# Kernel optimization log

Measured on AMD Instinct MI355X. Metric: run time of the kernel, lower is better.

## Reference

```python
import jax, jax.numpy as jnp
import numpy as np

N = 50000        # nodes
E = 800000       # edges
IN_FEAT = 128
OUT_FEAT = 64
HEADS = 4
NUM_CLASSES = 40
NEG_SLOPE = 0.2  # DGL GATConv default


def setup_inputs() -> dict:
    key = jax.random.key(0)
    ks = jax.random.split(key, 12)
    x = jax.random.normal(ks[0], (N, IN_FEAT), dtype=jnp.float32)
    src = jax.random.randint(ks[1], (E,), 0, N, dtype=jnp.int32)
    dst = jax.random.randint(ks[2], (E,), 0, N, dtype=jnp.int32)
    # layer 1 params: fc W1 [in, H*D], attn_l/attn_r [H, D], bias [H*D]
    s1 = 1.0 / np.sqrt(IN_FEAT)
    W1 = jax.random.normal(ks[3], (IN_FEAT, HEADS * OUT_FEAT), dtype=jnp.float32) * s1
    al1 = jax.random.normal(ks[4], (HEADS, OUT_FEAT), dtype=jnp.float32) * 0.1
    ar1 = jax.random.normal(ks[5], (HEADS, OUT_FEAT), dtype=jnp.float32) * 0.1
    b1 = jnp.zeros((HEADS * OUT_FEAT,), dtype=jnp.float32)
    # layer 2 params: fc W2 [H*D, C], attn [1, C], bias [C]
    hid = HEADS * OUT_FEAT
    s2 = 1.0 / np.sqrt(hid)
    W2 = jax.random.normal(ks[6], (hid, NUM_CLASSES), dtype=jnp.float32) * s2
    al2 = jax.random.normal(ks[7], (1, NUM_CLASSES), dtype=jnp.float32) * 0.1
    ar2 = jax.random.normal(ks[8], (1, NUM_CLASSES), dtype=jnp.float32) * 0.1
    b2 = jnp.zeros((NUM_CLASSES,), dtype=jnp.float32)
    return {"x": x, "src": src, "dst": dst,
            "W1": W1, "al1": al1, "ar1": ar1, "b1": b1,
            "W2": W2, "al2": al2, "ar2": ar2, "b2": b2}


def gat_layer(x, W, al, ar, bias, src, dst, heads, out_feat):
    n = x.shape[0]
    h = (x @ W).reshape(n, heads, out_feat)            # [N,H,D]
    el = jnp.sum(h * al[None], axis=-1)                # [N,H]
    er = jnp.sum(h * ar[None], axis=-1)                # [N,H]
    e = el[src] + er[dst]                              # [E,H]
    e = jnp.where(e > 0, e, NEG_SLOPE * e)             # LeakyReLU
    # segment softmax over edges sharing the same destination
    emax = jax.ops.segment_max(e, dst, num_segments=n)           # [N,H]
    emax = jnp.where(jnp.isfinite(emax), emax, 0.0)              # isolated nodes
    ee = jnp.exp(e - emax[dst])                                  # [E,H]
    denom = jax.ops.segment_sum(ee, dst, num_segments=n)         # [N,H]
    denom = jnp.where(denom > 0, denom, 1.0)
    alpha = ee / denom[dst]                                      # [E,H]
    msg = h[src] * alpha[:, :, None]                             # [E,H,D]
    out = jax.ops.segment_sum(msg, dst, num_segments=n)          # [N,H,D]
    return out + bias.reshape(1, heads, out_feat)


def reference(x, src, dst, W1, al1, ar1, b1, W2, al2, ar2, b2):
    h = gat_layer(x, W1, al1, ar1, b1, src, dst, HEADS, OUT_FEAT)  # [N,H,D]
    h = h.reshape(h.shape[0], HEADS * OUT_FEAT)
    h = jax.nn.elu(h)
    h = gat_layer(h, W2, al2, ar2, b2, src, dst, 1, NUM_CLASSES)   # [N,1,C]
    return jnp.squeeze(h, axis=1)                                   # [N,C]
```

## Files before the change

### kernel.cpp

```cpp
#include <hip/hip_runtime.h>

#define NN 50000
#define NE 800000
#define HID 256
#define NCLS 40

typedef short bf16x8 __attribute__((ext_vector_type(8)));
typedef float f32x4 __attribute__((ext_vector_type(4)));

__device__ inline unsigned short f2bf(float f) {
    unsigned int u = __float_as_uint(f);
    return (unsigned short)((u + 0x7FFFu + ((u >> 16) & 1u)) >> 16);
}
__device__ inline unsigned int pack2bf(float a, float b) {
    return (unsigned int)f2bf(a) | ((unsigned int)f2bf(b) << 16);
}
__device__ inline float2 bf2x(unsigned int u) {
    return make_float2(__uint_as_float(u << 16), __uint_as_float(u & 0xFFFF0000u));
}

__global__ void k_count(const int* __restrict__ dst, int* __restrict__ counts) {
    int e = blockIdx.x * 256 + threadIdx.x;
    if (e < NE) atomicAdd(&counts[dst[e]], 1);
}

__global__ void k_scanA(const int* __restrict__ counts, int* __restrict__ indptr,
                        int* __restrict__ bsum) {
    __shared__ int sh[256];
    int t = threadIdx.x;
    int idx = blockIdx.x * 256 + t;
    int c = idx < NN ? counts[idx] : 0;
    sh[t] = c;
    __syncthreads();
    for (int off = 1; off < 256; off <<= 1) {
        int v = (t >= off) ? sh[t - off] : 0;
        __syncthreads();
        sh[t] += v;
        __syncthreads();
    }
    if (idx < NN) indptr[idx] = sh[t] - c;
    if (t == 255) bsum[blockIdx.x] = sh[255];
}

__global__ void k_scanB(int* __restrict__ bsum, int nb) {
    __shared__ int sh[256];
    int t = threadIdx.x;
    int c = t < nb ? bsum[t] : 0;
    sh[t] = c;
    __syncthreads();
    for (int off = 1; off < 256; off <<= 1) {
        int v = (t >= off) ? sh[t - off] : 0;
        __syncthreads();
        sh[t] += v;
        __syncthreads();
    }
    if (t < nb) bsum[t] = sh[t] - c;
}

__global__ void k_scanC(int* __restrict__ indptr, const int* __restrict__ bsum,
                        int* __restrict__ fill) {
    int idx = blockIdx.x * 256 + threadIdx.x;
    if (idx < NN) {
        indptr[idx] += bsum[idx >> 8];
        fill[idx] = 0;
    }
    if (idx == 0) indptr[NN] = NE;
}

__global__ void k_scatterw(const int* __restrict__ src, const int* __restrict__ dst,
                           const int* __restrict__ indptr, int* __restrict__ fill,
                           const float* __restrict__ el1, const float* __restrict__ er1,
                           int* __restrict__ srcs, float4* __restrict__ w4) {
    int e = blockIdx.x * 256 + threadIdx.x;
    if (e < NE) {
        int d = dst[e];
        int s = src[e];
        int pos = atomicAdd(&fill[d], 1);
        int j = indptr[d] + pos;
        srcs[j] = s;
        float4 ls = *(const float4*)&el1[(size_t)s * 4];
        float4 rd = *(const float4*)&er1[(size_t)d * 4];
        float e0 = ls.x + rd.x, e1 = ls.y + rd.y, e2 = ls.z + rd.z, e3 = ls.w + rd.w;
        e0 = e0 > 0.f ? e0 : 0.2f * e0;
        e1 = e1 > 0.f ? e1 : 0.2f * e1;
        e2 = e2 > 0.f ? e2 : 0.2f * e2;
        e3 = e3 > 0.f ? e3 : 0.2f * e3;
        w4[j] = make_float4(__expf(e0), __expf(e1), __expf(e2), __expf(e3));
    }
}

__global__ void k_prep(const float* __restrict__ W1, const float* __restrict__ al,
                       const float* __restrict__ ar, const float* __restrict__ W2,
                       float* __restrict__ wel, float* __restrict__ wer,
                       unsigned short* __restrict__ W1Tb,
                       unsigned short* __restrict__ W2Tb) {
    int gid = blockIdx.x * 256 + threadIdx.x;
    int nth = gridDim.x * 256;
    const int TOT = 512 + 32768 + 48 * 256;
    for (int i = gid; i < TOT; i += nth) {
        if (i < 512) {
            int k = i >> 2, h = i & 3;
            float a = 0.f, b = 0.f;
            for (int dd = 0; dd < 64; ++dd) {
                float w = W1[k * 256 + h * 64 + dd];
                a = fmaf(w, al[h * 64 + dd], a);
                b = fmaf(w, ar[h * 64 + dd], b);
            }
            wel[i] = a;
            wer[i] = b;
        } else if (i < 512 + 32768) {
            int j = i - 512;
            int col = j >> 7, k = j & 127;
            W1Tb[j] = f2bf(W1[k * 256 + col]);
        } else {
            int j = i - 512 - 32768;
            int col = j >> 8, kk = j & 255;
            W2Tb[j] = (col < NCLS) ? f2bf(W2[kk * 40 + col]) : (unsigned short)0;
        }
    }
}

__global__ void k_elr1x(const float* __restrict__ x, const float* __restrict__ wel,
                        const float* __restrict__ wer, float* __restrict__ el1,
                        float* __restrict__ er1, unsigned short* __restrict__ xb) {
    __shared__ float xs[64 * 129];
    __shared__ float wels[512], wers[512];
    int t = threadIdx.x;
    int n0 = blockIdx.x * 64;
    wels[t] = wel[t]; wels[256 + t] = wel[256 + t];
    wers[t] = wer[t]; wers[256 + t] = wer[256 + t];
    for (int i = 0; i < 8; ++i) {
        int f = i * 256 + t;
        int row = f >> 5;
        int col4 = (f & 31) * 4;
        float4 v = make_float4(0.f, 0.f, 0.f, 0.f);
        if (n0 + row < NN) v = ((const float4*)x)[(size_t)n0 * 32 + f];
        xs[row * 129 + col4 + 0] = v.x;
        xs[row * 129 + col4 + 1] = v.y;
        xs[row * 129 + col4 + 2] = v.z;
        xs[row * 129 + col4 + 3] = v.w;
    }
    __syncthreads();
    int node = t & 63;
    int h = t >> 6;
    float a = 0.f, b = 0.f;
    for (int k = 0; k < 128; ++k) {
        float xv = xs[node * 129 + k];
        a = fmaf(xv, wels[k * 4 + h], a);
        b = fmaf(xv, wers[k * 4 + h], b);
    }
    if (n0 + node < NN) {
        el1[(size_t)(n0 + node) * 4 + h] = a;
        er1[(size_t)(n0 + node) * 4 + h] = b;
    }
    for (int i = 0; i < 4; ++i) {
        int g = (i * 256 + t) * 8;
        int row = g >> 7, col = g & 127;
        if (n0 + row < NN) {
            ushort4 lo, hi;
            lo.x = f2bf(xs[row * 129 + col + 0]);
            lo.y = f2bf(xs[row * 129 + col + 1]);
            lo.z = f2bf(xs[row * 129 + col + 2]);
            lo.w = f2bf(xs[row * 129 + col + 3]);
            hi.x = f2bf(xs[row * 129 + col + 4]);
            hi.y = f2bf(xs[row * 129 + col + 5]);
            hi.z = f2bf(xs[row * 129 + col + 6]);
            hi.w = f2bf(xs[row * 129 + col + 7]);
            *(ushort4*)&xb[(size_t)(n0 + row) * 128 + col] = lo;
            *(ushort4*)&xb[(size_t)(n0 + row) * 128 + col + 4] = hi;
        }
    }
}

#define XG_STRIDE 260
#define EB_STRIDE 264
#define FMA8(AC0, AC1, AC2, AC3, WQ, XV) \
    AC0.x = fmaf(WQ.x, XV.x, AC0.x); AC0.y = fmaf(WQ.x, XV.y, AC0.y); \
    AC1.x = fmaf(WQ.y, XV.x, AC1.x); AC1.y = fmaf(WQ.y, XV.y, AC1.y); \
    AC2.x = fmaf(WQ.z, XV.x, AC2.x); AC2.y = fmaf(WQ.z, XV.y, AC2.y); \
    AC3.x = fmaf(WQ.w, XV.x, AC3.x); AC3.y = fmaf(WQ.w, XV.y, AC3.y);

__global__ void k_agg1m(const unsigned int* __restrict__ xb32,
                        const float4* __restrict__ w4,
                        const int* __restrict__ indptr, const int* __restrict__ srcs,
                        const unsigned short* __restrict__ W1Tb,
                        const unsigned short* __restrict__ W2Tb,
                        const float* __restrict__ b1,
                        const float* __restrict__ al2, const float* __restrict__ ar2,
                        unsigned short* __restrict__ h2b,
                        float* __restrict__ el2, float* __restrict__ er2) {
    __shared__ unsigned int xg[16 * XG_STRIDE];
    __shared__ __align__(16) unsigned char pool[10496];
    float4 (*sw)[64] = (float4(*)[64])pool;
    int (*si)[64] = (int(*)[64])(pool + 8192);
    unsigned short* eb = (unsigned short*)pool;
    float* pel = (float*)(pool + 8448);
    float* per_ = (float*)(pool + 8640);
    int t = threadIdx.x;
    int wv = t >> 6, l = t & 63;
    int n0 = blockIdx.x * 16;
    int d0 = n0 + wv * 4;
    int ip[5];
#pragma unroll
    for (int q = 0; q < 5; ++q) ip[q] = indptr[d0 + q];
    int w2 = wv * 2;
#pragma unroll
    for (int p = 0; p < 2; ++p) {
        int begA = ip[2 * p + 0], endA = ip[2 * p + 1];
        int begB = ip[2 * p + 1], endB = ip[2 * p + 2];
        int degA = endA - begA, degB = endB - begB;
        int sA = 0, sB = 0;
        float4 wA = make_float4(0.f, 0.f, 0.f, 0.f);
        float4 wB = make_float4(0.f, 0.f, 0.f, 0.f);
        if (l < degA) { sA = srcs[begA + l]; wA = w4[begA + l]; }
        if (l < degB) { sB = srcs[begB + l]; wB = w4[begB + l]; }
        si[w2 + 0][l] = sA; sw[w2 + 0][l] = wA;
        si[w2 + 1][l] = sB; sw[w2 + 1][l] = wB;
        float2 aA0 = {0,0}, aA1 = {0,0}, aA2 = {0,0}, aA3 = {0,0};
        float2 aB0 = {0,0}, aB1 = {0,0}, aB2 = {0,0}, aB3 = {0,0};
        int capA = degA < 64 ? degA : 64;
        int capB = degB < 64 ? degB : 64;
        int mcap = capA > capB ? capA : capB;
        for (int e = 0; e < mcap; e += 8) {
            unsigned int uA[8], uB[8];
            bool doA = e < capA, doB = e < capB;
            if (doA) {
#pragma unroll
                for (int q = 0; q < 8; ++q)
                    uA[q] = xb32[(size_t)si[w2][e + q] * 64 + l];
            }
            if (doB) {
#pragma unroll
                for (int q = 0; q < 8; ++q)
                    uB[q] = xb32[(size_t)si[w2 + 1][e + q] * 64 + l];
            }
            if (doA) {
#pragma unroll
                for (int q = 0; q < 8; ++q) {
                    float4 wq = sw[w2][e + q];
                    float2 xv = bf2x(uA[q]);
                    FMA8(aA0, aA1, aA2, aA3, wq, xv)
                }
            }
            if (doB) {
#pragma unroll
                for (int q = 0; q < 8; ++q) {
                    float4 wq = sw[w2 + 1][e + q];
                    float2 xv = bf2x(uB[q]);
                    FMA8(aB0, aB1, aB2, aB3, wq, xv)
                }
            }
        }
        for (int j = begA + 64; j < endA; ++j) {
            float4 wq = w4[j];
            float2 xv = bf2x(xb32[(size_t)srcs[j] * 64 + l]);
            FMA8(aA0, aA1, aA2, aA3, wq, xv)
        }
        for (int j = begB + 64; j < endB; ++j) {
            float4 wq = w4[j];
            float2 xv = bf2x(xb32[(size_t)srcs[j] * 64 + l]);
            FMA8(aB0, aB1, aB2, aB3, wq, xv)
        }
        float dA0 = wA.x, dA1 = wA.y, dA2 = wA.z, dA3 = wA.w;
        float dB0 = wB.x, dB1 = wB.y, dB2 = wB.z, dB3 = wB.w;
        for (int j = begA + 64 + l; j < endA; j += 64) {
            float4 wt = w4[j];
            dA0 += wt.x; dA1 += wt.y; dA2 += wt.z; dA3 += wt.w;
        }
        for (int j = begB + 64 + l; j < endB; j += 64) {
            float4 wt = w4[j];
            dB0 += wt.x; dB1 += wt.y; dB2 += wt.z; dB3 += wt.w;
        }
#pragma unroll
        for (int off = 32; off > 0; off >>= 1) {
            dA0 += __shfl_xor(dA0, off); dA1 += __shfl_xor(dA1, off);
            dA2 += __shfl_xor(dA2, off); dA3 += __shfl_xor(dA3, off);
            dB0 += __shfl_xor(dB0, off); dB1 += __shfl_xor(dB1, off);
            dB2 += __shfl_xor(dB2, off); dB3 += __shfl_xor(dB3, off);
        }
        float iA0 = dA0 > 0.f ? 1.f / dA0 : 0.f;
        float iA1 = dA1 > 0.f ? 1.f / dA1 : 0.f;
        float iA2 = dA2 > 0.f ? 1.f / dA2 : 0.f;
        float iA3 = dA3 > 0.f ? 1.f / dA3 : 0.f;
        float iB0 = dB0 > 0.f ? 1.f / dB0 : 0.f;
        float iB1 = dB1 > 0.f ? 1.f / dB1 : 0.f;
        float iB2 = dB2 > 0.f ? 1.f / dB2 : 0.f;
        float iB3 = dB3 > 0.f ? 1.f / dB3 : 0.f;
        unsigned int* xgA = &xg[(wv * 4 + 2 * p + 0) * XG_STRIDE];
        xgA[0 * 64 + l] = pack2bf(aA0.x * iA0, aA0.y * iA0);
        xgA[1 * 64 + l] = pack2bf(aA1.x * iA1, aA1.y * iA1);
        xgA[2 * 64 + l] = pack2bf(aA2.x * iA2, aA2.y * iA2);
        xgA[3 * 64 + l] = pack2bf(aA3.x * iA3, aA3.y * iA3);
        unsigned int* xgB = &xg[(wv * 4 + 2 * p + 1) * XG_STRIDE];
        xgB[0 * 64 + l] = pack2bf(aB0.x * iB0, aB0.y * iB0);
        xgB[1 * 64 + l] = pack2bf(aB1.x * iB1, aB1.y * iB1);
        xgB[2 * 64 + l] = pack2bf(aB2.x * iB2, aB2.y * iB2);
        xgB[3 * 64 + l] = pack2bf(aB3.x * iB3, aB3.y * iB3);
    }
    __syncthreads();
    int lrow = l & 15, lk = l >> 4;
    {
        f32x4 acc[4] = {};
#pragma unroll
        for (int kt = 0; kt < 4; ++kt) {
            bf16x8 av = *(const bf16x8*)&xg[lrow * XG_STRIDE + wv * 64 + kt * 16 + lk * 4];
#pragma unroll
            for (int nt = 0; nt < 4; ++nt) {
                int col = wv * 64 + nt * 16 + lrow;
                bf16x8 bv = *(const bf16x8*)&W1Tb[(size_t)col * 128 + kt * 32 + lk * 8];
                acc[nt] = __builtin_amdgcn_mfma_f32_16x16x32_bf16(av, bv, acc[nt], 0, 0, 0);
            }
        }
#pragma unroll
        for (int nt = 0; nt < 4; ++nt) {
            int col = wv * 64 + nt * 16 + lrow;
            float bv1 = b1[col];
#pragma unroll
            for (int r = 0; r < 4; ++r) {
                int rloc = lk * 4 + r;
                float o = acc[nt][r] + bv1;
                o = o > 0.f ? o : (__expf(o) - 1.f);
                eb[rloc * EB_STRIDE + col] = f2bf(o);
            }
        }
    }
    __syncthreads();
    if (wv < 3) {
        f32x4 acc2 = {};
#pragma unroll
        for (int kt = 0; kt < 8; ++kt) {
            bf16x8 av = *(const bf16x8*)&eb[lrow * EB_STRIDE + kt * 32 + lk * 8];
            bf16x8 bv = *(const bf16x8*)&W2Tb[(size_t)(wv * 16 + lrow) * 256 + kt * 32 + lk * 8];
            acc2 = __builtin_amdgcn_mfma_f32_16x16x32_bf16(av, bv, acc2, 0, 0, 0);
        }
        int col2 = wv * 16 + lrow;
        float alc = col2 < NCLS ? al2[col2] : 0.f;
        float arc = col2 < NCLS ? ar2[col2] : 0.f;
#pragma unroll
        for (int r = 0; r < 4; ++r) {
            int row = n0 + lk * 4 + r;
            float v = acc2[r];
            if (col2 < NCLS) h2b[(size_t)row * NCLS + col2] = f2bf(v);
            float pa = v * alc, pb = v * arc;
#pragma unroll
            for (int off = 1; off < 16; off <<= 1) {
                pa += __shfl_xor(pa, off);
                pb += __shfl_xor(pb, off);
            }
            if (lrow == 0) {
                pel[wv * 16 + lk * 4 + r] = pa;
                per_[wv * 16 + lk * 4 + r] = pb;
            }
        }
    }
    __syncthreads();
    if (t < 16) {
        el2[n0 + t] = pel[t] + pel[16 + t] + pel[32 + t];
        er2[n0 + t] = per_[t] + per_[16 + t] + per_[32 + t];
    }
}

__global__ void k_agg2(const unsigned int* __restrict__ h2b32,
                       const float* __restrict__ el2,
                       const float* __restrict__ er2, const float* __restrict__ b2,
                       const int* __restrict__ indptr, const int* __restrict__ srcs,
                       float* __restrict__ out) {
    __shared__ int   si[8][64];
    __shared__ float sw[8][64];
    int t = threadIdx.x;
    int wv = t >> 6, l = t & 63;
    int dA = blockIdx.x * 8 + wv * 2;
    int dB = dA + 1;
    int begA = indptr[dA], endA = indptr[dA + 1];
    int begB = endA, endB = indptr[dB + 1];
    int degA = endA - begA, degB = endB - begB;
    float rdA = er2[dA], rdB = er2[dB];
    int sA = 0, sB = 0;
    float wA = 0.f, wB = 0.f;
    if (l < degA) {
        sA = srcs[begA + l];
        float e = el2[sA] + rdA;
        e = e > 0.f ? e : 0.2f * e;
        wA = __expf(e);
    }
    if (l < degB) {
        sB = srcs[begB + l];
        float e = el2[sB] + rdB;
        e = e > 0.f ? e : 0.2f * e;
        wB = __expf(e);
    }
    int w2 = wv * 2;
    si[w2 + 0][l] = sA; sw[w2 + 0][l] = wA;
    si[w2 + 1][l] = sB; sw[w2 + 1][l] = wB;
    float denA = wA, denB = wB;
    for (int j = begA + 64 + l; j < endA; j += 64) {
        float e = el2[srcs[j]] + rdA;
        e = e > 0.f ? e : 0.2f * e;
        denA += __expf(e);
    }
    for (int j = begB + 64 + l; j < endB; j += 64) {
        float e = el2[srcs[j]] + rdB;
        e = e > 0.f ? e : 0.2f * e;
        denB += __expf(e);
    }
    int half = l >> 5, il = l & 31;
    bool act = il < 20;
    float2 accA = {0.f, 0.f}, accB = {0.f, 0.f};
    int capA = degA < 64 ? degA : 64;
    int capB = degB < 64 ? degB : 64;
    int mcap = capA > capB ? capA : capB;
    for (int e = 0; e < mcap; e += 8) {
        bool doA = e < capA, doB = e < capB;
        int ixA[4], ixB[4];
        float wsA[4], wsB[4];
        unsigned int uA[4], uB[4];
        if (doA) {
#pragma unroll
            for (int q = 0; q < 4; ++q) {
                int idx = e + 2 * q + half;
                ixA[q] = si[w2][idx];
                wsA[q] = sw[w2][idx];
            }
        }
        if (doB) {
#pragma unroll
            for (int q = 0; q < 4; ++q) {
                int idx = e + 2 * q + half;
                ixB[q] = si[w2 + 1][idx];
                wsB[q] = sw[w2 + 1][idx];
            }
        }
        if (doA) {
#pragma unroll
            for (int q = 0; q < 4; ++q)
                uA[q] = act ? h2b32[(size_t)ixA[q] * 20 + il] : 0u;
        }
        if (doB) {
#pragma unroll
            for (int q = 0; q < 4; ++q)
                uB[q] = act ? h2b32[(size_t)ixB[q] * 20 + il] : 0u;
        }
        if (doA) {
#pragma unroll
            for (int q = 0; q < 4; ++q) {
                float2 xv = bf2x(uA[q]);
                accA.x = fmaf(wsA[q], xv.x, accA.x);
                accA.y = fmaf(wsA[q], xv.y, accA.y);
            }
        }
        if (doB) {
#pragma unroll
            for (int q = 0; q < 4; ++q) {
                float2 xv = bf2x(uB[q]);
                accB.x = fmaf(wsB[q], xv.x, accB.x);
                accB.y = fmaf(wsB[q], xv.y, accB.y);
            }
        }
    }
    for (int j = begA + 64; j < endA; ++j) {
        int s = srcs[j];
        float e = el2[s] + rdA;
        e = e > 0.f ? e : 0.2f * e;
        float ww = (half == 0) ? __expf(e) : 0.f;
        unsigned int u = act ? h2b32[(size_t)s * 20 + il] : 0u;
        float2 xv = bf2x(u);
        accA.x = fmaf(ww, xv.x, accA.x);
        accA.y = fmaf(ww, xv.y, accA.y);
    }
    for (int j = begB + 64; j < endB; ++j) {
        int s = srcs[j];
        float e = el2[s] + rdB;
        e = e > 0.f ? e : 0.2f * e;
        float ww = (half == 0) ? __expf(e) : 0.f;
        unsigned int u = act ? h2b32[(size_t)s * 20 + il] : 0u;
        float2 xv = bf2x(u);
        accB.x = fmaf(ww, xv.x, accB.x);
        accB.y = fmaf(ww, xv.y, accB.y);
    }
#pragma unroll
    for (int off = 32; off > 0; off >>= 1) {
        denA += __shfl_xor(denA, off);
        denB += __shfl_xor(denB, off);
    }
    float invA = denA > 0.f ? 1.f / denA : 0.f;
    float invB = denB > 0.f ? 1.f / denB : 0.f;
    accA.x += __shfl_xor(accA.x, 32);
    accA.y += __shfl_xor(accA.y, 32);
    accB.x += __shfl_xor(accB.x, 32);
    accB.y += __shfl_xor(accB.y, 32);
    if (half == 0 && act) {
        float2 bb = *(const float2*)&b2[2 * il];
        *(float2*)&out[(size_t)dA * NCLS + 2 * il] =
            make_float2(fmaf(accA.x, invA, bb.x), fmaf(accA.y, invA, bb.y));
        *(float2*)&out[(size_t)dB * NCLS + 2 * il] =
            make_float2(fmaf(accB.x, invB, bb.x), fmaf(accB.y, invB, bb.y));
    }
}

extern "C" void kernel_launch(void* const* d_in, const int* in_sizes, int n_in,
                              void* d_out, int out_size, void* d_ws, size_t ws_size,
                              hipStream_t stream) {
    const float* x   = (const float*)d_in[0];
    const int*   src = (const int*)d_in[1];
    const int*   dst = (const int*)d_in[2];
    const float* W1  = (const float*)d_in[3];
    const float* al1 = (const float*)d_in[4];
    const float* ar1 = (const float*)d_in[5];
    const float* b1  = (const float*)d_in[6];
    const float* W2  = (const float*)d_in[7];
    const float* al2 = (const float*)d_in[8];
    const float* ar2 = (const float*)d_in[9];
    const float* b2  = (const float*)d_in[10];
    float* out = (float*)d_out;

    float* ws = (float*)d_ws;
    size_t off = 0;
    unsigned short* xb    = (unsigned short*)(ws + off); off += (size_t)NN * 64;
    unsigned short* h2b   = (unsigned short*)(ws + off); off += (size_t)NN * 20;
    float* el1  = ws + off; off += (size_t)NN * 4;
    float* er1  = ws + off; off += (size_t)NN * 4;
    float* el2  = ws + off; off += NN;
    float* er2  = ws + off; off += NN;
    float* wel  = ws + off; off += 512;
    float* wer  = ws + off; off += 512;
    unsigned short* w1tb = (unsigned short*)(ws + off); off += 16384;
    unsigned short* w2tb = (unsigned short*)(ws + off); off += 48 * 128;
    float* w4   = ws + off; off += (size_t)NE * 4;
    int* counts = (int*)(ws + off);
    int* indptr = counts + NN;
    int* fill   = indptr + NN + 1;
    int* srcs   = fill + NN;
    int* bsum   = srcs + NE;

    const int NB = (NN + 255) / 256;

    hipMemsetAsync(counts, 0, NN * sizeof(int), stream);

    k_count<<<(NE + 255) / 256, 256, 0, stream>>>(dst, counts);
    k_scanA<<<NB, 256, 0, stream>>>(counts, indptr, bsum);
    k_scanB<<<1, 256, 0, stream>>>(bsum, NB);
    k_scanC<<<NB, 256, 0, stream>>>(indptr, bsum, fill);

    k_prep<<<48, 256, 0, stream>>>(W1, al1, ar1, W2, wel, wer, w1tb, w2tb);
    k_elr1x<<<(NN + 63) / 64, 256, 0, stream>>>(x, wel, wer, el1, er1, xb);
    k_scatterw<<<(NE + 255) / 256, 256, 0, stream>>>(src, dst, indptr, fill,
                                                     el1, er1, srcs, (float4*)w4);
    k_agg1m<<<NN / 16, 256, 0, stream>>>((const unsigned int*)xb, (const float4*)w4,
                                         indptr, srcs, w1tb, w2tb, b1, al2, ar2,
                                         h2b, el2, er2);

    k_agg2<<<NN / 8, 256, 0, stream>>>((const unsigned int*)h2b, el2, er2, b2,
                                       indptr, srcs, out);
}
```

Before: 206.8 us.

## Fuse degree counting into elr1x and halve nodes per agg1m block

The edge-count atomics move into the tail of k_elr1x as a grid-stride loop, which removes the separate k_count launch and reorders launches so prep and elr1x run before the scan. k_agg1m now handles 8 destination nodes per block instead of 16, doubling the grid and shrinking shared memory per block. The MFMA tiles stay 16 rows, so half of each tile is duplicate work that gets discarded. This trades wasted matrix work and less per-block amortisation for more blocks and better latency hiding in the gather phase.

```diff
diff --git a/kernel.cpp b/kernel.cpp
--- a/kernel.cpp
+++ b/kernel.cpp
@@ -17,11 +17,6 @@
 }
 __device__ inline float2 bf2x(unsigned int u) {
     return make_float2(__uint_as_float(u << 16), __uint_as_float(u & 0xFFFF0000u));
-}
-
-__global__ void k_count(const int* __restrict__ dst, int* __restrict__ counts) {
-    int e = blockIdx.x * 256 + threadIdx.x;
-    if (e < NE) atomicAdd(&counts[dst[e]], 1);
 }
 
 __global__ void k_scanA(const int* __restrict__ counts, int* __restrict__ indptr,
@@ -122,7 +117,8 @@
 
 __global__ void k_elr1x(const float* __restrict__ x, const float* __restrict__ wel,
                         const float* __restrict__ wer, float* __restrict__ el1,
-                        float* __restrict__ er1, unsigned short* __restrict__ xb) {
+                        float* __restrict__ er1, unsigned short* __restrict__ xb,
+                        const int* __restrict__ dst, int* __restrict__ counts) {
     __shared__ float xs[64 * 129];
     __shared__ float wels[512], wers[512];
     int t = threadIdx.x;
@@ -170,6 +166,9 @@
             *(ushort4*)&xb[(size_t)(n0 + row) * 128 + col + 4] = hi;
         }
     }
+    int gid = blockIdx.x * 256 + t;
+    int nth = gridDim.x * 256;
+    for (int e = gid; e < NE; e += nth) atomicAdd(&counts[dst[e]], 1);
 }
 
 #define XG_STRIDE 260
@@ -189,25 +188,22 @@
                         const float* __restrict__ al2, const float* __restrict__ ar2,
                         unsigned short* __restrict__ h2b,
                         float* __restrict__ el2, float* __restrict__ er2) {
-    __shared__ unsigned int xg[16 * XG_STRIDE];
+    __shared__ unsigned int xg[8 * XG_STRIDE];
     __shared__ __align__(16) unsigned char pool[10496];
     float4 (*sw)[64] = (float4(*)[64])pool;
     int (*si)[64] = (int(*)[64])(pool + 8192);
     unsigned short* eb = (unsigned short*)pool;
-    float* pel = (float*)(pool + 8448);
-    float* per_ = (float*)(pool + 8640);
+    float* pel = (float*)(pool + 4224);
+    float* per_ = (float*)(pool + 4320);
     int t = threadIdx.x;
     int wv = t >> 6, l = t & 63;
-    int n0 = blockIdx.x * 16;
-    int d0 = n0 + wv * 4;
-    int ip[5];
-#pragma unroll
-    for (int q = 0; q < 5; ++q) ip[q] = indptr[d0 + q];
+    int n0 = blockIdx.x * 8;
+    int d0 = n0 + wv * 2;
+    int ip0 = indptr[d0], ip1 = indptr[d0 + 1], ip2 = indptr[d0 + 2];
     int w2 = wv * 2;
-#pragma unroll
-    for (int p = 0; p < 2; ++p) {
-        int begA = ip[2 * p + 0], endA = ip[2 * p + 1];
-        int begB = ip[2 * p + 1], endB = ip[2 * p + 2];
+    {
+        int begA = ip0, endA = ip1;
+        int begB = ip1, endB = ip2;
         int degA = endA - begA, degB = endB - begB;
         int sA = 0, sB = 0;
         float4 wA = make_float4(0.f, 0.f, 0.f, 0.f);
@@ -286,12 +282,12 @@
         float iB1 = dB1 > 0.f ? 1.f / dB1 : 0.f;
         float iB2 = dB2 > 0.f ? 1.f / dB2 : 0.f;
         float iB3 = dB3 > 0.f ? 1.f / dB3 : 0.f;
-        unsigned int* xgA = &xg[(wv * 4 + 2 * p + 0) * XG_STRIDE];
+        unsigned int* xgA = &xg[(w2 + 0) * XG_STRIDE];
         xgA[0 * 64 + l] = pack2bf(aA0.x * iA0, aA0.y * iA0);
         xgA[1 * 64 + l] = pack2bf(aA1.x * iA1, aA1.y * iA1);
         xgA[2 * 64 + l] = pack2bf(aA2.x * iA2, aA2.y * iA2);
         xgA[3 * 64 + l] = pack2bf(aA3.x * iA3, aA3.y * iA3);
-        unsigned int* xgB = &xg[(wv * 4 + 2 * p + 1) * XG_STRIDE];
+        unsigned int* xgB = &xg[(w2 + 1) * XG_STRIDE];
         xgB[0 * 64 + l] = pack2bf(aB0.x * iB0, aB0.y * iB0);
         xgB[1 * 64 + l] = pack2bf(aB1.x * iB1, aB1.y * iB1);
         xgB[2 * 64 + l] = pack2bf(aB2.x * iB2, aB2.y * iB2);
@@ -300,10 +296,11 @@
     __syncthreads();
     int lrow = l & 15, lk = l >> 4;
     {
+        int arow = lrow & 7;
         f32x4 acc[4] = {};
 #pragma unroll
         for (int kt = 0; kt < 4; ++kt) {
-            bf16x8 av = *(const bf16x8*)&xg[lrow * XG_STRIDE + wv * 64 + kt * 16 + lk * 4];
+            bf16x8 av = *(const bf16x8*)&xg[arow * XG_STRIDE + wv * 64 + kt * 16 + lk * 4];
 #pragma unroll
             for (int nt = 0; nt < 4; ++nt) {
                 int col = wv * 64 + nt * 16 + lrow;
@@ -311,25 +308,28 @@
                 acc[nt] = __builtin_amdgcn_mfma_f32_16x16x32_bf16(av, bv, acc[nt], 0, 0, 0);
             }
         }
-#pragma unroll
-        for (int nt = 0; nt < 4; ++nt) {
-            int col = wv * 64 + nt * 16 + lrow;
-            float bv1 = b1[col];
-#pragma unroll
-            for (int r = 0; r < 4; ++r) {
-                int rloc = lk * 4 + r;
-                float o = acc[nt][r] + bv1;
-                o = o > 0.f ? o : (__expf(o) - 1.f);
-                eb[rloc * EB_STRIDE + col] = f2bf(o);
+        if (lk < 2) {
+#pragma unroll
+            for (int nt = 0; nt < 4; ++nt) {
+                int col = wv * 64 + nt * 16 + lrow;
+                float bv1 = b1[col];
+#pragma unroll
+                for (int r = 0; r < 4; ++r) {
+                    int rloc = lk * 4 + r;
+                    float o = acc[nt][r] + bv1;
+                    o = o > 0.f ? o : (__expf(o) - 1.f);
+                    eb[rloc * EB_STRIDE + col] = f2bf(o);
+                }
             }
         }
     }
     __syncthreads();
     if (wv < 3) {
+        int arow = lrow & 7;
         f32x4 acc2 = {};
 #pragma unroll
         for (int kt = 0; kt < 8; ++kt) {
-            bf16x8 av = *(const bf16x8*)&eb[lrow * EB_STRIDE + kt * 32 + lk * 8];
+            bf16x8 av = *(const bf16x8*)&eb[arow * EB_STRIDE + kt * 32 + lk * 8];
             bf16x8 bv = *(const bf16x8*)&W2Tb[(size_t)(wv * 16 + lrow) * 256 + kt * 32 + lk * 8];
             acc2 = __builtin_amdgcn_mfma_f32_16x16x32_bf16(av, bv, acc2, 0, 0, 0);
         }
@@ -338,25 +338,28 @@
         float arc = col2 < NCLS ? ar2[col2] : 0.f;
 #pragma unroll
         for (int r = 0; r < 4; ++r) {
-            int row = n0 + lk * 4 + r;
+            int rloc = lk * 4 + r;
             float v = acc2[r];
-            if (col2 < NCLS) h2b[(size_t)row * NCLS + col2] = f2bf(v);
             float pa = v * alc, pb = v * arc;
 #pragma unroll
             for (int off = 1; off < 16; off <<= 1) {
                 pa += __shfl_xor(pa, off);
                 pb += __shfl_xor(pb, off);
             }
-            if (lrow == 0) {
-                pel[wv * 16 + lk * 4 + r] = pa;
-                per_[wv * 16 + lk * 4 + r] = pb;
+            if (rloc < 8) {
+                int row = n0 + rloc;
+                if (col2 < NCLS) h2b[(size_t)row * NCLS + col2] = f2bf(v);
+                if (lrow == 0) {
+                    pel[wv * 8 + rloc] = pa;
+                    per_[wv * 8 + rloc] = pb;
+                }
             }
         }
     }
     __syncthreads();
-    if (t < 16) {
-        el2[n0 + t] = pel[t] + pel[16 + t] + pel[32 + t];
-        er2[n0 + t] = per_[t] + per_[16 + t] + per_[32 + t];
+    if (t < 8) {
+        el2[n0 + t] = pel[t] + pel[8 + t] + pel[16 + t];
+        er2[n0 + t] = per_[t] + per_[8 + t] + per_[16 + t];
     }
 }
 
@@ -536,18 +539,16 @@
 
     hipMemsetAsync(counts, 0, NN * sizeof(int), stream);
 
-    k_count<<<(NE + 255) / 256, 256, 0, stream>>>(dst, counts);
+    k_prep<<<48, 256, 0, stream>>>(W1, al1, ar1, W2, wel, wer, w1tb, w2tb);
+    k_elr1x<<<(NN + 63) / 64, 256, 0, stream>>>(x, wel, wer, el1, er1, xb, dst, counts);
     k_scanA<<<NB, 256, 0, stream>>>(counts, indptr, bsum);
     k_scanB<<<1, 256, 0, stream>>>(bsum, NB);
     k_scanC<<<NB, 256, 0, stream>>>(indptr, bsum, fill);
-
-    k_prep<<<48, 256, 0, stream>>>(W1, al1, ar1, W2, wel, wer, w1tb, w2tb);
-    k_elr1x<<<(NN + 63) / 64, 256, 0, stream>>>(x, wel, wer, el1, er1, xb);
     k_scatterw<<<(NE + 255) / 256, 256, 0, stream>>>(src, dst, indptr, fill,
                                                      el1, er1, srcs, (float4*)w4);
-    k_agg1m<<<NN / 16, 256, 0, stream>>>((const unsigned int*)xb, (const float4*)w4,
-                                         indptr, srcs, w1tb, w2tb, b1, al2, ar2,
-                                         h2b, el2, er2);
+    k_agg1m<<<NN / 8, 256, 0, stream>>>((const unsigned int*)xb, (const float4*)w4,
+                                        indptr, srcs, w1tb, w2tb, b1, al2, ar2,
+                                        h2b, el2, er2);
 
     k_agg2<<<NN / 8, 256, 0, stream>>>((const unsigned int*)h2b, el2, er2, b2,
                                        indptr, srcs, out);
```

Result: slower. 224.2 us (+8.4%).
